# Kernel optimization log

Measured on AMD Instinct MI355X. Metric: run time of the kernel, lower is better.

Reference implementation:

```python
import jax, jax.numpy as jnp
import numpy as np

A, C, V, G = 100000, 230, 800, 60          # athletes, countries, events, games
H, HEADS, DH = 128, 4, 32                   # hidden, gat heads, per-head dim (H = HEADS*DH)
E_AC, E_AE, E_AG, E_EG = 100000, 500000, 300000, 2000
NEG_SLOPE = 0.2


def _seg_mean(msg, idx, n):
    s = jax.ops.segment_sum(msg, idx, num_segments=n)
    cnt = jax.ops.segment_sum(jnp.ones((idx.shape[0], 1), msg.dtype), idx, num_segments=n)
    return s / jnp.maximum(cnt, 1.0)


def _sage(xs, xd, ei, Wl, bl, Wr):
    # PyG SAGEConv(mean): lin_l(mean_neighbors) + lin_r(x_dst); bias lives in lin_l
    agg = _seg_mean(xs[ei[0]], ei[1], xd.shape[0])
    return agg @ Wl + bl + xd @ Wr


def _gatv2(xs, xd, ei, Wl, bl, Wr, br, att, bias):
    # PyG GATv2Conv, concat=True, add_self_loops=False, eval mode (no dropout)
    n = xd.shape[0]
    xl = (xs @ Wl + bl).reshape(-1, HEADS, DH)   # [Ns,H,d]
    xr = (xd @ Wr + br).reshape(-1, HEADS, DH)   # [Nd,H,d]
    src, dst = ei[0], ei[1]
    e = jax.nn.leaky_relu(xl[src] + xr[dst], NEG_SLOPE)      # [E,H,d]
    logit = jnp.einsum('ehd,hd->eh', e, att)                 # [E,H]
    m = jax.ops.segment_max(logit, dst, num_segments=n)
    m = jnp.where(jnp.isneginf(m), 0.0, m)                   # empty dst segments
    ex = jnp.exp(logit - m[dst])
    den = jax.ops.segment_sum(ex, dst, num_segments=n)
    alpha = ex / (den[dst] + 1e-16)
    out = jax.ops.segment_sum(xl[src] * alpha[:, :, None], dst, num_segments=n)
    return out.reshape(n, HEADS * DH) + bias


def _mlp(x, W1, b1, W2, b2):
    return jax.nn.relu(x @ W1 + b1) @ W2 + b2


def _forward(x_athlete, x_country, x_event, x_games,
             eAW1, eAb1, eAW2, eAb2, eCW1, eCb1, eCW2, eCb2,
             eEW1, eEb1, eEW2, eEb2, eGW1, eGb1, eGW2, eGb2,
             sage_Wl, sage_bl, sage_Wr,
             gat_Wl, gat_bl, gat_Wr, gat_br, gat_att, gat_bias,
             ei_ac, ei_ae, ei_ag, ei_eg):
    x = {
        'athlete': _mlp(x_athlete, eAW1, eAb1, eAW2, eAb2),
        'country': _mlp(x_country, eCW1, eCb1, eCW2, eCb2),
        'event':   _mlp(x_event,   eEW1, eEb1, eEW2, eEb2),
        'games':   _mlp(x_games,   eGW1, eGb1, eGW2, eGb2),
    }
    rev = lambda ei: ei[::-1]
    etypes = [
        ('athlete', 'country', ei_ac), ('country', 'athlete', rev(ei_ac)),
        ('athlete', 'event',   ei_ae), ('event',   'athlete', rev(ei_ae)),
        ('athlete', 'games',   ei_ag), ('games',   'athlete', rev(ei_ag)),
        ('event',   'games',   ei_eg), ('games',   'event',   rev(ei_eg)),
    ]
    # layer 1: hetero SAGEConv, HeteroConv aggr='mean' over edge types per dst
    outs = {t: [] for t in x}
    for k, (s, d, ei) in enumerate(etypes):
        outs[d].append(_sage(x[s], x[d], ei, sage_Wl[k], sage_bl[k], sage_Wr[k]))
    x = {t: jax.nn.relu(sum(o) / len(o)) for t, o in outs.items()}
    # layer 2 (final): hetero GATv2Conv, mean over edge types per dst
    outs = {t: [] for t in x}
    for k, (s, d, ei) in enumerate(etypes):
        outs[d].append(_gatv2(x[s], x[d], ei, gat_Wl[k], gat_bl[k], gat_Wr[k],
                              gat_br[k], gat_att[k], gat_bias[k]))
    x = {t: sum(o) / len(o) for t, o in outs.items()}
    return jnp.concatenate([x['athlete'], x['country'], x['event'], x['games']], axis=0)


def setup_inputs() -> dict:
    key = jax.random.key(0)
    ks = iter(jax.random.split(key, 80))
    def nrm(shape, scale=1.0):
        return jax.random.normal(next(ks), shape, jnp.float32) * scale
    def lin(fi, fo):
        return nrm((fi, fo), 1.0 / np.sqrt(fi))
    def edges(ns, nd, E):
        s = jax.random.randint(next(ks), (E,), 0, ns)
        d = jax.random.randint(next(ks), (E,), 0, nd)
        return jnp.stack([s, d]).astype(jnp.int32)
    sc = 1.0 / np.sqrt(H)
    return {
        'x_athlete': nrm((A, 7)), 'x_country': nrm((C, 3)),
        'x_event': nrm((V, 384)), 'x_games': nrm((G, 2)),
        'ei_ac': edges(A, C, E_AC), 'ei_ae': edges(A, V, E_AE),
        'ei_ag': edges(A, G, E_AG), 'ei_eg': edges(V, G, E_EG),
        'eAW1': lin(7, H),   'eAb1': jnp.zeros((H,)), 'eAW2': lin(H, H), 'eAb2': jnp.zeros((H,)),
        'eCW1': lin(3, H),   'eCb1': jnp.zeros((H,)), 'eCW2': lin(H, H), 'eCb2': jnp.zeros((H,)),
        'eEW1': lin(384, H), 'eEb1': jnp.zeros((H,)), 'eEW2': lin(H, H), 'eEb2': jnp.zeros((H,)),
        'eGW1': lin(2, H),   'eGb1': jnp.zeros((H,)), 'eGW2': lin(H, H), 'eGb2': jnp.zeros((H,)),
        'sage_Wl': nrm((8, H, H), sc), 'sage_bl': jnp.zeros((8, H)), 'sage_Wr': nrm((8, H, H), sc),
        'gat_Wl': nrm((8, H, H), sc), 'gat_bl': jnp.zeros((8, H)),
        'gat_Wr': nrm((8, H, H), sc), 'gat_br': jnp.zeros((8, H)),
        'gat_att': nrm((8, HEADS, DH), 1.0 / np.sqrt(DH)), 'gat_bias': jnp.zeros((8, H)),
    }


def reference(x_athlete, x_country, x_event, x_games,
              eAW1, eAb1, eAW2, eAb2, eCW1, eCb1, eCW2, eCb2,
              eEW1, eEb1, eEW2, eEb2, eGW1, eGb1, eGW2, eGb2,
              sage_Wl, sage_bl, sage_Wr,
              gat_Wl, gat_bl, gat_Wr, gat_br, gat_att, gat_bias,
              ei_ac, ei_ae, ei_ag, ei_eg):
    return _forward(x_athlete, x_country, x_event, x_games,
                    eAW1, eAb1, eAW2, eAb2, eCW1, eCb1, eCW2, eCb2,
                    eEW1, eEb1, eEW2, eEb2, eGW1, eGb1, eGW2, eGb2,
                    sage_Wl, sage_bl, sage_Wr,
                    gat_Wl, gat_bl, gat_Wr, gat_br, gat_att, gat_bias,
                    ei_ac, ei_ae, ei_ag, ei_eg)
```

## Files before the change

kernel.cpp:

```cpp
#include <hip/hip_runtime.h>
#include <hip/hip_bf16.h>

#define A_N 100000
#define C_N 230
#define V_N 800
#define G_N 60

#define FLAG_RELU 2

#define SCAN_N   302080
#define SCAN_NB  295
#define E_TOTAL  1804000

#define PCHUNK 16

typedef __attribute__((ext_vector_type(8))) short short8;
typedef __attribute__((ext_vector_type(4))) float f32x4;

__device__ __forceinline__ float bf16dec(unsigned short u){
  return __uint_as_float(((unsigned)u) << 16);
}
__device__ __forceinline__ unsigned short f2b(float v){
  union { __hip_bfloat16 h; unsigned short u; } c;
  c.h = __float2bfloat16(v);
  return c.u;
}
__device__ __forceinline__ float4 ldb4(const unsigned short* p){
  uint2 v = *(const uint2*)p;
  float4 r;
  r.x = __uint_as_float(v.x << 16);
  r.y = __uint_as_float(v.x & 0xffff0000u);
  r.z = __uint_as_float(v.y << 16);
  r.w = __uint_as_float(v.y & 0xffff0000u);
  return r;
}
static inline int imin(int a, int b){ return a < b ? a : b; }

__global__ void detect_dtype(const unsigned short* __restrict__ p, int* __restrict__ flag){
  __shared__ int bad;
  if (threadIdx.x == 0) bad = 0;
  __syncthreads();
  for (int i = threadIdx.x; i < 2048; i += blockDim.x){
    float v = fabsf(bf16dec(p[i]));
    if (!(v <= 1e6f)) atomicOr(&bad, 1);
  }
  __syncthreads();
  if (threadIdx.x == 0) *flag = bad;
}

struct ConvTab { const void* src[29]; int dstoff[29]; int cum[30]; };

__global__ void convert_all(ConvTab tab, float* __restrict__ wsf,
                            const int* __restrict__ flagp, int total){
  const int f = *flagp;
  for (int idx = blockIdx.x*blockDim.x + threadIdx.x; idx < total;
       idx += gridDim.x*blockDim.x){
    int t = 0;
    while (idx >= tab.cum[t+1]) ++t;
    int l = idx - tab.cum[t];
    float v = f ? ((const float*)tab.src[t])[l]
                : bf16dec(((const unsigned short*)tab.src[t])[l]);
    wsf[tab.dstoff[t] + l] = v;
  }
}

__global__ void prep_combos(const float* __restrict__ sWr, const float* __restrict__ sbl,
                            const float* __restrict__ gbias,
                            const float* __restrict__ gbl, const float* __restrict__ gbr,
                            float* __restrict__ wrcomb, float* __restrict__ sbcomb,
                            float* __restrict__ gbcomb,
                            float* __restrict__ gblx, float* __restrict__ gbrx){
  const int sets[4][3] = {{1,3,5},{0,-1,-1},{2,7,-1},{4,6,-1}};
  const float inv[4] = {1.f/3.f, 1.f, 0.5f, 0.5f};
  int idx = blockIdx.x*blockDim.x + threadIdx.x;
  if (idx >= 4*16384) return;
  int t = idx >> 14, j = idx & 16383;
  float s = 0.f;
  #pragma unroll
  for (int q = 0; q < 3; ++q){
    int k = sets[t][q];
    if (k >= 0) s += sWr[k*16384 + j];
  }
  wrcomb[idx] = s * inv[t];
  if (j < 128){
    float b1 = 0.f, b2 = 0.f;
    #pragma unroll
    for (int q = 0; q < 3; ++q){
      int k = sets[t][q];
      if (k >= 0){ b1 += sbl[k*128 + j]; b2 += gbias[k*128 + j]; }
    }
    sbcomb[t*128 + j] = b1 * inv[t];
    gbcomb[t*128 + j] = b2 * inv[t];
  }
  if (idx < 384){
    const int kl[3] = {0,2,4}, kr[3] = {1,3,5};
    int rel = idx >> 7, jj = idx & 127;
    gblx[idx] = gbl[kl[rel]*128 + jj];
// ... 155 lines not shown
__global__ void enc_batch(const float* __restrict__ wsf, unsigned short* __restrict__ wsu,
                          EncTab t){
  for (int idx = blockIdx.x*blockDim.x + threadIdx.x; idx < t.cum[4];
       idx += gridDim.x*blockDim.x){
    int s = 0;
    while (idx >= t.cum[s+1]) ++s;
    int local = idx - t.cum[s];
    if (s < 3){
      int r = local >> 7, c = local & 127;
      int K = t.K[s];
      float acc = wsf[t.boff[s] + c];
      for (int k = 0; k < K; ++k)
        acc = fmaf(wsf[t.xoff[s] + r*K + k], wsf[t.woff[s] + (k<<7) + c], acc);
      wsu[(size_t)t.zoff[s] + (size_t)r*128 + c] = f2b(fmaxf(acc, 0.f));
    } else {
      wsu[(size_t)t.zoff[3] + local] = f2b(wsf[t.xoff[3] + local]);
    }
  }
}

__device__ __forceinline__ void mfma_core(
    const unsigned short* __restrict__ wsu, const float* __restrict__ wsf,
    int xoff, int xstride, int x2off, int x2stride, int kcsplit,
    int woff, int nkc, int biasoff, int yoff, int ystride,
    int M, int flags, int mblk, int nblk)
{
  int tid = threadIdx.x;
  int wv = tid >> 6, lane = tid & 63;
  int quad = lane >> 4, ml = lane & 15;
  int m0 = mblk*64 + wv*16;
  if (m0 >= M) return;
  int arow = m0 + ml;
  bool rowok = arow < M;
  f32x4 acc[8];
  #pragma unroll
  for (int i = 0; i < 8; ++i) acc[i] = (f32x4){0.f, 0.f, 0.f, 0.f};
  for (int kc = 0; kc < nkc; ++kc){
    short8 a = (short8){0,0,0,0,0,0,0,0};
    if (rowok){
      size_t ao = (kc < kcsplit)
        ? (size_t)xoff  + (size_t)arow*xstride  + kc*32 + quad*8
        : (size_t)x2off + (size_t)arow*x2stride + (kc - kcsplit)*32 + quad*8;
      a = *(const short8*)(wsu + ao);
    }
    size_t wbase = (size_t)woff + ((size_t)(nblk*8)*nkc + kc)*512 + lane*8;
    #pragma unroll
    for (int nt = 0; nt < 8; ++nt){
      short8 b = *(const short8*)(wsu + wbase + (size_t)nt*nkc*512);
      acc[nt] = __builtin_amdgcn_mfma_f32_16x16x32_bf16(a, b, acc[nt], 0, 0, 0);
    }
  }
  #pragma unroll
  for (int nt = 0; nt < 8; ++nt){
    int col = nblk*128 + nt*16 + ml;
    float bv = (biasoff >= 0) ? wsf[biasoff + col] : 0.f;
    #pragma unroll
    for (int r = 0; r < 4; ++r){
      int orow = m0 + quad*4 + r;
      if (orow < M){
        float v = acc[nt][r] + bv;
        if (flags & FLAG_RELU) v = fmaxf(v, 0.f);
        *((unsigned short*)wsu + (size_t)yoff + (size_t)orow*ystride + col) = f2b(v);
      }
    }
  }
}

struct GB2 { int xoff, xstride, x2off, x2stride, kcsplit, woff, nkc, biasoff,
             yoff, ystride, M, flags, nblk; };
struct GB2Tab { GB2 d[13]; int b0[14]; int n; };

__global__ __launch_bounds__(256) void mfma_gemm_b2(void* ws, GB2Tab t){
  int b = blockIdx.x, di = 0;
  while (b >= t.b0[di+1]) ++di;
  GB2 g = t.d[di];
  mfma_core((const unsigned short*)ws, (const float*)ws, g.xoff, g.xstride,
            g.x2off, g.x2stride, g.kcsplit, g.woff, g.nkc, g.biasoff,
            g.yoff, g.ystride, g.M, g.flags, b - t.b0[di], g.nblk);
}

struct SgD { int src, sstr, rpoff, aggoff, nd, nc; };
struct SgTab { SgD d[5]; int cumw[6]; };

__global__ void sage_all(const unsigned short* __restrict__ wsu, float* __restrict__ wsf,
    const int* __restrict__ csr, const int* __restrict__ rpb, SgTab t,
    int uhC, int uhE, int uhG, int rp1, int rp3, int rp5, int uagg)
{
  int gid = (blockIdx.x*blockDim.x + threadIdx.x) >> 6;
  int lane = threadIdx.x & 63;
  int half = lane >> 5, sub = lane & 31, f = sub*4;
  if (gid < A_N){
    int srcs[3] = {uhC, uhE, uhG};
    int sstr[3] = {256, 384, 384};
    int rps[3]  = {rp1, rp3, rp5};
    #pragma unroll
    for (int rel = 0; rel < 3; ++rel){
      const unsigned short* base = wsu + (size_t)srcs[rel] + f;
      int str = sstr[rel];
      int st = rpb[rps[rel] + gid], en = rpb[rps[rel] + gid + 1];
      float4 acc = {0.f, 0.f, 0.f, 0.f};
      int i = st + half;
      for (; i + 2 < en; i += 4){
        int s0 = csr[i], s1 = csr[i+2];
        float4 v0 = ldb4(base + (size_t)s0*str);
        float4 v1 = ldb4(base + (size_t)s1*str);
        acc.x += v0.x + v1.x; acc.y += v0.y + v1.y;
        acc.z += v0.z + v1.z; acc.w += v0.w + v1.w;
      }
      if (i < en){
        float4 v0 = ldb4(base + (size_t)csr[i]*str);
        acc.x += v0.x; acc.y += v0.y; acc.z += v0.z; acc.w += v0.w;
      }
      acc.x += __shfl_xor(acc.x, 32); acc.y += __shfl_xor(acc.y, 32);
      acc.z += __shfl_xor(acc.z, 32); acc.w += __shfl_xor(acc.w, 32);
      if (half == 0){
        int deg = en - st;
        float sc = 1.f / (float)(deg > 1 ? deg : 1);
        ushort4 o;
        o.x = f2b(acc.x*sc); o.y = f2b(acc.y*sc);
        o.z = f2b(acc.z*sc); o.w = f2b(acc.w*sc);
        *(ushort4*)((unsigned short*)wsu + (size_t)uagg + (size_t)gid*384 + rel*128 + f) = o;
      }
    }
  } else {
    int wid = gid - A_N;
    if (wid >= t.cumw[5]) return;
    int di = 0;
    while (wid >= t.cumw[di+1]) ++di;
    SgD d = t.d[di];
    int local = wid - t.cumw[di];
    int row = local / d.nc, c = local - row*d.nc;
    const unsigned short* base = wsu + (size_t)d.src + f;
    int st = rpb[d.rpoff + row], en = rpb[d.rpoff + row + 1];
    float4 acc = {0.f, 0.f, 0.f, 0.f};
    int i = st + c + half*d.nc;
    int step = 2*d.nc;
    for (; i + step < en; i += 2*step){
      int s0 = csr[i], s1 = csr[i+step];
      float4 v0 = ldb4(base + (size_t)s0*d.sstr);
      float4 v1 = ldb4(base + (size_t)s1*d.sstr);
      acc.x += v0.x + v1.x; acc.y += v0.y + v1.y;
      acc.z += v0.z + v1.z; acc.w += v0.w + v1.w;
    }
    if (i < en){
      float4 v0 = ldb4(base + (size_t)csr[i]*d.sstr);
      acc.x += v0.x; acc.y += v0.y; acc.z += v0.z; acc.w += v0.w;
    }
    acc.x += __shfl_xor(acc.x, 32); acc.y += __shfl_xor(acc.y, 32);
    acc.z += __shfl_xor(acc.z, 32); acc.w += __shfl_xor(acc.w, 32);
    if (half == 0){
      float* o = wsf + (size_t)d.aggoff + (size_t)row*128 + f;
      atomicAdd(o,   acc.x); atomicAdd(o+1, acc.y);
      atomicAdd(o+2, acc.z); atomicAdd(o+3, acc.w);
    }
  }
}

struct AfD { int aggoff, rpoff, dstu, dstr, nd; };
struct AfTab { AfD d[5]; int n; };

__global__ void aggfin_batch(unsigned short* __restrict__ wsu, const float* __restrict__ wsf,
                             const int* __restrict__ rpb, AfTab t, int total){
  int idx = blockIdx.x*blockDim.x + threadIdx.x;
  if (idx >= total) return;
  int di = 0, local = idx;
  while (local >= t.d[di].nd*128){ local -= t.d[di].nd*128; ++di; }
  AfD d = t.d[di];
  int row = local >> 7, col = local & 127;
  int deg = rpb[d.rpoff + row + 1] - rpb[d.rpoff + row];
  float sc = 1.f / (float)(deg > 1 ? deg : 1);
  wsu[(size_t)d.dstu + (size_t)row*d.dstr + col] = f2b(wsf[(size_t)d.aggoff + local] * sc);
}

#define GAT_LOGIT(xv, pout)                                                \
  {                                                                        \
    float e0 = (xv).x + xrv.x, e1 = (xv).y + xrv.y;                        \
    float e2 = (xv).z + xrv.z, e3 = (xv).w + xrv.w;                        \
    e0 = e0 > 0.f ? e0 : 0.2f*e0; e1 = e1 > 0.f ? e1 : 0.2f*e1;            \
    e2 = e2 > 0.f ? e2 : 0.2f*e2; e3 = e3 > 0.f ? e3 : 0.2f*e3;            \
    pout = e0*av.x + e1*av.y + e2*av.z + e3*av.w;                          \
    pout += __shfl_xor(pout, 1); pout += __shfl_xor(pout, 2);              \
    pout += __shfl_xor(pout, 4);                                           \
  }

#define GAT_UPD(xv)                                                        \
  {                                                                        \
    float p;                                                               \
    GAT_LOGIT(xv, p);                                                      \
    float nm = fmaxf(m, p);                                                \
    float scw = __expf(m - nm);                                            \
    float pe = __expf(p - nm);                                             \
    l = l*scw + pe;                                                        \
    acc.x = acc.x*scw + pe*(xv).x; acc.y = acc.y*scw + pe*(xv).y;          \
    acc.z = acc.z*scw + pe*(xv).z; acc.w = acc.w*scw + pe*(xv).w;          \
    m = nm;                                                                \
  }

#define GAT_UPD2(x0, x1)                                                   \
  {                                                                        \
    float p0, p1;                                                          \
    GAT_LOGIT(x0, p0);                                                     \
    GAT_LOGIT(x1, p1);                                                     \
    float nm = fmaxf(m, fmaxf(p0, p1));                                    \
    float scw = __expf(m - nm);                                            \
    float pe0 = __expf(p0 - nm);                                           \
    float pe1 = __expf(p1 - nm);                                           \
    l = l*scw + pe0 + pe1;                                                 \
    acc.x = acc.x*scw + pe0*(x0).x + pe1*(x1).x;                           \
    acc.y = acc.y*scw + pe0*(x0).y + pe1*(x1).y;                           \
    acc.z = acc.z*scw + pe0*(x0).z + pe1*(x1).z;                           \
    acc.w = acc.w*scw + pe0*(x0).w + pe1*(x1).w;                           \
    m = nm;                                                                \
  }

#define GAT_MERGE_HALVES                                                   \
  {                                                                        \
    float mo = __shfl_xor(m, 32);                                          \
    float lo = __shfl_xor(l, 32);                                          \
    float4 ao;                                                             \
    ao.x = __shfl_xor(acc.x, 32); ao.y = __shfl_xor(acc.y, 32);            \
    ao.z = __shfl_xor(acc.z, 32); ao.w = __shfl_xor(acc.w, 32);            \
    float nm = fmaxf(m, mo);                                               \
    float w  = (m  == -INFINITY) ? 0.f : __expf(m  - nm);                  \
    float wo = (mo == -INFINITY) ? 0.f : __expf(mo - nm);                  \
    l = l*w + lo*wo;                                                       \
    acc.x = acc.x*w + ao.x*wo; acc.y = acc.y*w + ao.y*wo;                  \
    acc.z = acc.z*w + ao.z*wo; acc.w = acc.w*w + ao.w*wo;                  \
    m = nm;                                                                \
  }

__global__ void gat_ath(const unsigned short* __restrict__ wsu, const float* __restrict__ wsf,
    const int* __restrict__ csr, const int* __restrict__ rpb,
    int ugxr, int uxl1, int uxl3, int uxl5, int oatt, int rp1, int rp3, int rp5, int uout)
{
  int gid = (blockIdx.x*blockDim.x + threadIdx.x) >> 6;
  if (gid >= A_N) return;
  int lane = threadIdx.x & 63;
  int half = lane >> 5, sub = lane & 31, f = sub*4;
  int xls[3] = {uxl1, uxl3, uxl5};
  int rps[3] = {rp1, rp3, rp5};
  const int attk[3] = {1, 3, 5};
  float4 oacc = {0.f, 0.f, 0.f, 0.f};
  #pragma unroll
  for (int rel = 0; rel < 3; ++rel){
    float4 xrv = ldb4(wsu + (size_t)ugxr + (size_t)gid*384 + rel*128 + f);
    float4 av  = *(const float4*)(wsf + oatt + attk[rel]*128 + f);
    const unsigned short* base = wsu + (size_t)xls[rel] + f;
    int st = rpb[rps[rel] + gid], en = rpb[rps[rel] + gid + 1];
    float m = -INFINITY, l = 0.f;
    float4 acc = {0.f, 0.f, 0.f, 0.f};
    int i = st + half;
    for (; i + 2 < en; i += 4){
      int s0 = csr[i], s1 = csr[i+2];
      float4 x0 = ldb4(base + (size_t)s0*128);
      float4 x1 = ldb4(base + (size_t)s1*128);
      GAT_UPD2(x0, x1);
    }
    if (i < en){
      float4 x0 = ldb4(base + (size_t)csr[i]*128);
      GAT_UPD(x0);
    }
    GAT_MERGE_HALVES;
    float inv = 1.f / (l + 1e-16f);
    oacc.x += acc.x * inv; oacc.y += acc.y * inv;
    oacc.z += acc.z * inv; oacc.w += acc.w * inv;
  }
  if (half == 0){
    ushort4 o;
    o.x = f2b(oacc.x * (1.f/3.f)); o.y = f2b(oacc.y * (1.f/3.f));
    o.z = f2b(oacc.z * (1.f/3.f)); o.w = f2b(oacc.w * (1.f/3.f));
    *(ushort4*)((unsigned short*)wsu + (size_t)uout + (size_t)gid*128 + f) = o;
  }
}

struct GoD { int xl, xlstr, xr, attoff, rpoff, prefix, nd, nc; };
struct GoTab { GoD d[5]; int cumw[6]; };

__global__ void gat_online_batch(const unsigned short* __restrict__ wsu,
    const float* __restrict__ wsf, const int* __restrict__ csr,
    const int* __restrict__ rpb, float* __restrict__ part, GoTab t)
{
  int gid = (blockIdx.x*blockDim.x + threadIdx.x) >> 6;
  if (gid >= t.cumw[5]) return;
  int di = 0;
  while (gid >= t.cumw[di+1]) ++di;
  GoD d = t.d[di];
  int local = gid - t.cumw[di];
  int row = local / d.nc, c = local - row*d.nc;
  int lane = threadIdx.x & 63;
  int half = lane >> 5, sub = lane & 31, f = sub*4, h = sub >> 3;
  float4 xrv = ldb4(wsu + (size_t)d.xr + (size_t)row*128 + f);
  float4 av  = *(const float4*)(wsf + d.attoff + f);
  const unsigned short* base = wsu + (size_t)d.xl + f;
  int st = rpb[d.rpoff + row], en = rpb[d.rpoff + row + 1];
  float m = -INFINITY, l = 0.f;
  float4 acc = {0.f, 0.f, 0.f, 0.f};
  int i = st + c + half*d.nc;
  int step = 2*d.nc;
  for (; i + step < en; i += 2*step){
    int s0 = csr[i], s1 = csr[i+step];
    float4 x0 = ldb4(base + (size_t)s0*d.xlstr);
    float4 x1 = ldb4(base + (size_t)s1*d.xlstr);
    GAT_UPD2(x0, x1);
  }
  if (i < en){
    float4 x0 = ldb4(base + (size_t)csr[i]*d.xlstr);
    GAT_UPD(x0);
  }
  GAT_MERGE_HALVES;
  if (half == 0){
    float* pr = part + (size_t)(d.prefix + local)*136;
    if ((sub & 7) == 0){ pr[h] = m; pr[4+h] = l; }
    *(float4*)(pr + 8 + f) = acc;
  }
}

struct MgD { int prefix, outoff, nd, nc; float invS; };
struct MgTab { MgD d[5]; int cumw[6]; };

__global__ void gat_merge_batch(const float* __restrict__ part, float* __restrict__ wsf,
                                MgTab t){
  int gid = (blockIdx.x*blockDim.x + threadIdx.x) >> 6;
  if (gid >= t.cumw[5]) return;
  int di = 0;
  while (gid >= t.cumw[di+1]) ++di;
  MgD d = t.d[di];
  int row = gid - t.cumw[di];
  int lane = threadIdx.x & 63, f = lane*2, h = lane >> 4;
  float M = -INFINITY;
  for (int c = 0; c < d.nc; ++c)
    M = fmaxf(M, part[(size_t)(d.prefix + row*d.nc + c)*136 + h]);
  float L = 0.f;
  float2 acc = {0.f, 0.f};
  for (int c = 0; c < d.nc; ++c){
    const float* pr = part + (size_t)(d.prefix + row*d.nc + c)*136;
    float mc = pr[h];
    float w = (mc == -INFINITY) ? 0.f : __expf(mc - M);
    L += pr[4+h] * w;
    acc.x += pr[8+f]   * w;
    acc.y += pr[8+f+1] * w;
  }
  float inv = d.invS / (L + 1e-16f);
  float* o = wsf + (size_t)d.outoff + (size_t)row*128 + f;
  o[0] = acc.x * inv;
  o[1] = acc.y * inv;
}

__global__ void final_out(const unsigned short* __restrict__ wsu,
  const float* __restrict__ wsf, int uoutA, int oC0, int oE2, int oE7, int oG4, int oG6,
  int ogb, const int* __restrict__ flagp, void* __restrict__ dout)
{
  const int fl = *flagp;
  int idx = blockIdx.x*blockDim.x + threadIdx.x;
  const int total = 101090*128;
// ... 165 lines not shown
  for (int i = 0; i < 5; ++i) push(o_gWl + xlk[i]*16384, 128, u_smW[i], 4, 0, 0, 1.f);
  const int xrk[5] = {0,2,4,6,7};
  for (int i = 0; i < 5; ++i) push(o_gWr + xrk[i]*16384, 128, u_smW[5+i], 4, 0, 0, 1.f);
  st.n = sn; st.total = stotal;
  swz_batch<<<(stotal + 255)/256, 256, 0, stream>>>(wsf, wsu, st);

  hipMemsetAsync(wsf + o_cnt, 0, (size_t)SCAN_N*4, stream);
  {
    HTab ht; PTab pt;
    int hb = 0, pb = 0;
    for (int k = 0; k < 8; ++k){
      int E = et_E[k], nd = n_nodes[et_dst[k]];
      int small = (nd <= 800);
      ht.dp[k] = edp[k]; ht.E[k] = E; ht.cntoff[k] = rowbase[k];
      ht.ndst[k] = nd; ht.mode[k] = small;
      ht.bstart[k] = hb;
      hb += small ? imin(128, (E + 255)/256) : (E + 255)/256;
      pt.sp[k] = esp[k]; pt.dp[k] = edp[k]; pt.E[k] = E;
      pt.woffoff[k] = rowbase[k]; pt.ndst[k] = nd; pt.mode[k] = small;
      pt.bstart[k] = pb;
      pb += small ? imin(128, (E + 256*PCHUNK - 1)/(256*PCHUNK)) : (E + 255)/256;
    }
    ht.bstart[8] = hb; pt.bstart[8] = pb;
    hist_all<<<hb, 256, 0, stream>>>(ht, (int*)(wsf + o_cnt));
    scan1<<<SCAN_NB, 256, 0, stream>>>((int*)(wsf + o_cnt), rpb_p, (int*)(wsf + o_bsum));
    scan2<<<1, 512, 0, stream>>>((int*)(wsf + o_bsum));
    scan3<<<(SCAN_N + 255)/256, 256, 0, stream>>>(rpb_p, (int*)(wsf + o_woff),
                                                  (int*)(wsf + o_bsum));
    place_all<<<pb, 256, 0, stream>>>(pt, (int*)(wsf + o_woff), csr_p);
  }

  {
    EncTab et2;
    et2.cum[0] = 0;
    et2.cum[1] = A_N*128;
    et2.cum[2] = et2.cum[1] + C_N*128;
    et2.cum[3] = et2.cum[2] + G_N*128;
    et2.cum[4] = et2.cum[3] + 307200;
    et2.xoff[0] = coff[0]; et2.woff[0] = coff[4];  et2.boff[0] = coff[5];
    et2.zoff[0] = u_big0;  et2.K[0] = 7;
    et2.xoff[1] = coff[1]; et2.woff[1] = coff[8];  et2.boff[1] = coff[9];
    et2.zoff[1] = u_zC;    et2.K[1] = 3;
    et2.xoff[2] = coff[3]; et2.woff[2] = coff[16]; et2.boff[2] = coff[17];
    et2.zoff[2] = u_zG;    et2.K[2] = 2;
    et2.xoff[3] = coff[2]; et2.woff[3] = 0; et2.boff[3] = 0;
    et2.zoff[3] = u_xEb;   et2.K[3] = 0;
    enc_batch<<<(et2.cum[4] + 255)/256, 256, 0, stream>>>(wsf, wsu, et2);
  }

  auto pushG = [&](GB2Tab& T, GB2 g){
    T.d[T.n] = g;
    T.b0[T.n + 1] = T.b0[T.n] + (g.M + 63)/64;
    T.n++;
  };

  {
    GB2Tab t; t.n = 0; t.b0[0] = 0;
    pushG(t, GB2{u_zC, 128, 0,0,1000, u_eCW2, 4, coff[11], u_sxC, 256, C_N, 0, 0});
    pushG(t, GB2{u_xEb, 384, 0,0,1000, u_eEW1, 12, coff[13], u_zE, 128, V_N, FLAG_RELU, 0});
    pushG(t, GB2{u_zG, 128, 0,0,1000, u_eGW2, 4, coff[19], u_sxG, 384, G_N, 0, 0});
    pushG(t, GB2{u_big0, 128, 0,0,1000, u_eAW2, 4, coff[7], u_bigH, 128, A_N, 0, 0});
    mfma_gemm_b2<<<t.b0[t.n], 256, 0, stream>>>(d_ws, t);
  }
  {
    GB2Tab t; t.n = 0; t.b0[0] = 0;
    pushG(t, GB2{u_zE, 128, 0,0,1000, u_eEW2, 4, coff[15], u_sxE, 384, V_N, 0, 0});
    mfma_gemm_b2<<<t.b0[t.n], 256, 0, stream>>>(d_ws, t);
  }

  hipMemsetAsync(wsf + o_aggS, 0, (size_t)1950*128*4, stream);
  const int b0 = o_aggS, b2 = o_aggS + 230*128, b7 = b2 + 800*128,
            b4 = b7 + 800*128, b6 = b4 + 60*128;
  SgTab sg;
  sg.d[0] = SgD{u_bigH, 128, rowbase[0], b0, C_N, 32};
  sg.d[1] = SgD{u_bigH, 128, rowbase[2], b2, V_N, 16};
  sg.d[2] = SgD{u_sxG, 384, rowbase[7], b7, V_N, 8};
  sg.d[3] = SgD{u_bigH, 128, rowbase[4], b4, G_N, 128};
  sg.d[4] = SgD{u_sxE, 384, rowbase[6], b6, G_N, 32};
  sg.cumw[0] = 0;
  {
    int c = 0;
    for (int i = 0; i < 5; ++i){ c += sg.d[i].nd*sg.d[i].nc; sg.cumw[i+1] = c; }
  }
  {
    int waves = A_N + sg.cumw[5];
    sage_all<<<(waves*64 + 255)/256, 256, 0, stream>>>(wsu, wsf, csr_p, rpb_p, sg,
        u_sxC, u_sxE, u_sxG, rowbase[1], rowbase[3], rowbase[5], u_bigA);
  }
  AfTab af; af.n = 5;
  af.d[0] = AfD{b0, rowbase[0], u_sxC + 128, 256, C_N};
  af.d[1] = AfD{b2, rowbase[2], u_sxE + 128, 384, V_N};
  af.d[2] = AfD{b7, rowbase[7], u_sxE + 256, 384, V_N};
  af.d[3] = AfD{b4, rowbase[4], u_sxG + 128, 384, G_N};
  af.d[4] = AfD{b6, rowbase[6], u_sxG + 256, 384, G_N};
  int aftot = 1950*128;
  aggfin_batch<<<(aftot + 255)/256, 256, 0, stream>>>(wsu, wsf, rpb_p, af, aftot);

  {
    GB2Tab t; t.n = 0; t.b0[0] = 0;
    pushG(t, GB2{u_sxC, 256, 0,0,1000, u_sxCW, 8,  o_sbcomb + 128, u_yC, 128, C_N, FLAG_RELU, 0});
    pushG(t, GB2{u_sxE, 384, 0,0,1000, u_sxEW, 12, o_sbcomb + 256, u_yE, 128, V_N, FLAG_RELU, 0});
    pushG(t, GB2{u_sxG, 384, 0,0,1000, u_sxGW, 12, o_sbcomb + 384, u_yG, 128, G_N, FLAG_RELU, 0});
    pushG(t, GB2{u_bigH, 128, u_bigA, 384, 4, u_sxAW, 16, o_sbcomb, u_big0, 128, A_N, FLAG_RELU, 0});
    mfma_gemm_b2<<<t.b0[t.n], 256, 0, stream>>>(d_ws, t);
  }

  {
    GB2Tab t; t.n = 0; t.b0[0] = 0;
    pushG(t, GB2{u_big0, 128, 0,0,1000, u_gxlW, 4, o_gblx, u_bigA, 384, A_N, 0, 0});
    pushG(t, GB2{u_big0, 128, 0,0,1000, u_gxlW, 4, o_gblx, u_bigA, 384, A_N, 0, 1});
    pushG(t, GB2{u_big0, 128, 0,0,1000, u_gxlW, 4, o_gblx, u_bigA, 384, A_N, 0, 2});
    pushG(t, GB2{u_yC, 128, 0,0,1000, u_smW[0], 4, o_gbl + 1*128, u_xl1, 128, C_N, 0, 0});
    pushG(t, GB2{u_yE, 128, 0,0,1000, u_smW[1], 4, o_gbl + 3*128, u_xl3, 128, V_N, 0, 0});
    pushG(t, GB2{u_yG, 128, 0,0,1000, u_smW[2], 4, o_gbl + 5*128, u_xl5, 128, G_N, 0, 0});
    pushG(t, GB2{u_yE, 128, 0,0,1000, u_smW[3], 4, o_gbl + 6*128, u_xl6, 128, V_N, 0, 0});
    pushG(t, GB2{u_yG, 128, 0,0,1000, u_smW[4], 4, o_gbl + 7*128, u_xl7, 128, G_N, 0, 0});
    pushG(t, GB2{u_yC, 128, 0,0,1000, u_smW[5], 4, o_gbr + 0*128, u_xr0, 128, C_N, 0, 0});
    pushG(t, GB2{u_yE, 128, 0,0,1000, u_smW[6], 4, o_gbr + 2*128, u_xr2, 128, V_N, 0, 0});
    pushG(t, GB2{u_yG, 128, 0,0,1000, u_smW[7], 4, o_gbr + 4*128, u_xr4, 128, G_N, 0, 0});
    pushG(t, GB2{u_yG, 128, 0,0,1000, u_smW[8], 4, o_gbr + 6*128, u_xr6, 128, G_N, 0, 0});
    pushG(t, GB2{u_yE, 128, 0,0,1000, u_smW[9], 4, o_gbr + 7*128, u_xr7, 128, V_N, 0, 0});
    mfma_gemm_b2<<<t.b0[t.n], 256, 0, stream>>>(d_ws, t);
  }

  GoTab go;
  go.d[0] = GoD{u_bigA + 0,   384, u_xr0, o_gatt + 0*128, rowbase[0], 0,     C_N, 32};
  go.d[1] = GoD{u_bigA + 128, 384, u_xr2, o_gatt + 2*128, rowbase[2], 7360,  V_N, 16};
  go.d[2] = GoD{u_bigA + 256, 384, u_xr4, o_gatt + 4*128, rowbase[4], 20160, G_N, 128};
  go.d[3] = GoD{u_xl6, 128,        u_xr6, o_gatt + 6*128, rowbase[6], 27840, G_N, 32};
  go.d[4] = GoD{u_xl7, 128,        u_xr7, o_gatt + 7*128, rowbase[7], 29760, V_N, 8};
  go.cumw[0] = 0;
  {
    int c = 0;
    for (int i = 0; i < 5; ++i){ c += go.d[i].nd*go.d[i].nc; go.cumw[i+1] = c; }
  }
  gat_online_batch<<<(go.cumw[5]*64 + 255)/256, 256, 0, stream>>>(wsu, wsf, csr_p, rpb_p,
      wsf + o_part, go);

  {
    GB2Tab t; t.n = 0; t.b0[0] = 0;
    pushG(t, GB2{u_big0, 128, 0,0,1000, u_gxrW, 4, o_gbrx, u_bigA, 384, A_N, 0, 0});
    pushG(t, GB2{u_big0, 128, 0,0,1000, u_gxrW, 4, o_gbrx, u_bigA, 384, A_N, 0, 1});
    pushG(t, GB2{u_big0, 128, 0,0,1000, u_gxrW, 4, o_gbrx, u_bigA, 384, A_N, 0, 2});
    mfma_gemm_b2<<<t.b0[t.n], 256, 0, stream>>>(d_ws, t);
  }
  gat_ath<<<(A_N*64 + 255)/256, 256, 0, stream>>>(wsu, wsf, csr_p, rpb_p,
      u_bigA, u_xl1, u_xl3, u_xl5, o_gatt, rowbase[1], rowbase[3], rowbase[5], u_bigH);

  MgTab mg;
  mg.d[0] = MgD{0,     o_outC0, C_N, 32,  1.0f};
  mg.d[1] = MgD{7360,  o_outE2, V_N, 16,  0.5f};
  mg.d[2] = MgD{20160, o_outG4, G_N, 128, 0.5f};
  mg.d[3] = MgD{27840, o_outG6, G_N, 32,  0.5f};
  mg.d[4] = MgD{29760, o_outE7, V_N, 8,   0.5f};
  mg.cumw[0] = 0;
  {
    int c = 0;
    for (int i = 0; i < 5; ++i){ c += mg.d[i].nd; mg.cumw[i+1] = c; }
  }
  gat_merge_batch<<<(mg.cumw[5]*64 + 255)/256, 256, 0, stream>>>(wsf + o_part, wsf, mg);

  final_out<<<(101090*128 + 255)/256, 256, 0, stream>>>(wsu, wsf, u_bigH,
      o_outC0, o_outE2, o_outE7, o_outG4, o_outG6, o_gbcomb, flagp, d_out);
}
```

Measured before the change: 1.021 ms.

## Fuse athlete SAGE aggregation and GAT xr projection into their consumer kernels

The athlete-side SAGE mean aggregation now writes into LDS and is followed in the same kernel by the MFMA GEMM that produces the athlete hidden state. This avoids the global round trip through the aggregation buffer and the separate GEMM launch. Likewise, the GATv2 xr projection for athletes is computed per 64-row block into LDS inside the attention kernel rather than by a separate GEMM. The cost is one wave per 16 rows doing serial gathers, lower occupancy from about 50KB of LDS per block, and per-block reloading of the weights.

```diff
diff --git a/kernel.cpp b/kernel.cpp
--- a/kernel.cpp
+++ b/kernel.cpp
@@ -13,6 +13,7 @@
 #define E_TOTAL  1804000
 
 #define PCHUNK 16
+#define LROW 392
 
 typedef __attribute__((ext_vector_type(8))) short short8;
 typedef __attribute__((ext_vector_type(4))) float f32x4;
@@ -334,22 +335,81 @@
 struct SgD { int src, sstr, rpoff, aggoff, nd, nc; };
 struct SgTab { SgD d[5]; int cumw[6]; };
 
-__global__ void sage_all(const unsigned short* __restrict__ wsu, float* __restrict__ wsf,
-    const int* __restrict__ csr, const int* __restrict__ rpb, SgTab t,
-    int uhC, int uhE, int uhG, int rp1, int rp3, int rp5, int uagg)
+__global__ void sage_small(const unsigned short* __restrict__ wsu, float* __restrict__ wsf,
+    const int* __restrict__ csr, const int* __restrict__ rpb, SgTab t)
 {
   int gid = (blockIdx.x*blockDim.x + threadIdx.x) >> 6;
+  if (gid >= t.cumw[5]) return;
   int lane = threadIdx.x & 63;
   int half = lane >> 5, sub = lane & 31, f = sub*4;
-  if (gid < A_N){
-    int srcs[3] = {uhC, uhE, uhG};
-    int sstr[3] = {256, 384, 384};
-    int rps[3]  = {rp1, rp3, rp5};
+  int di = 0;
+  while (gid >= t.cumw[di+1]) ++di;
+  SgD d = t.d[di];
+  int local = gid - t.cumw[di];
+  int row = local / d.nc, c = local - row*d.nc;
+  const unsigned short* base = wsu + (size_t)d.src + f;
+  int st = rpb[d.rpoff + row], en = rpb[d.rpoff + row + 1];
+  float4 acc = {0.f, 0.f, 0.f, 0.f};
+  int i = st + c + half*d.nc;
+  int step = 2*d.nc;
+  for (; i + step < en; i += 2*step){
+    int s0 = csr[i], s1 = csr[i+step];
+    float4 v0 = ldb4(base + (size_t)s0*d.sstr);
+    float4 v1 = ldb4(base + (size_t)s1*d.sstr);
+    acc.x += v0.x + v1.x; acc.y += v0.y + v1.y;
+    acc.z += v0.z + v1.z; acc.w += v0.w + v1.w;
+  }
+  if (i < en){
+    float4 v0 = ldb4(base + (size_t)csr[i]*d.sstr);
+    acc.x += v0.x; acc.y += v0.y; acc.z += v0.z; acc.w += v0.w;
+  }
+  acc.x += __shfl_xor(acc.x, 32); acc.y += __shfl_xor(acc.y, 32);
+  acc.z += __shfl_xor(acc.z, 32); acc.w += __shfl_xor(acc.w, 32);
+  if (half == 0){
+    float* o = wsf + (size_t)d.aggoff + (size_t)row*128 + f;
+    atomicAdd(o,   acc.x); atomicAdd(o+1, acc.y);
+    atomicAdd(o+2, acc.z); atomicAdd(o+3, acc.w);
+  }
+}
+
+struct AfD { int aggoff, rpoff, dstu, dstr, nd; };
+struct AfTab { AfD d[5]; int n; };
+
+__global__ void aggfin_batch(unsigned short* __restrict__ wsu, const float* __restrict__ wsf,
+                             const int* __restrict__ rpb, AfTab t, int total){
+  int idx = blockIdx.x*blockDim.x + threadIdx.x;
+  if (idx >= total) return;
+  int di = 0, local = idx;
+  while (local >= t.d[di].nd*128){ local -= t.d[di].nd*128; ++di; }
+  AfD d = t.d[di];
+  int row = local >> 7, col = local & 127;
+  int deg = rpb[d.rpoff + row + 1] - rpb[d.rpoff + row];
+  float sc = 1.f / (float)(deg > 1 ? deg : 1);
+  wsu[(size_t)d.dstu + (size_t)row*d.dstr + col] = f2b(wsf[(size_t)d.aggoff + local] * sc);
+}
+
+__global__ __launch_bounds__(256) void sage_ath_fused(
+    unsigned short* __restrict__ wsu, const float* __restrict__ wsf,
+    const int* __restrict__ csr, const int* __restrict__ rpb,
+    int uhC, int uhE, int uhG, int rp1, int rp3, int rp5,
+    int uhA, int woff, int biasoff, int yoff)
+{
+  __shared__ unsigned short lds[64*LROW];
+  int tid = threadIdx.x;
+  int wv = tid >> 6, lane = tid & 63;
+  int half = lane >> 5, sub = lane & 31, f = sub*4;
+  int m0 = blockIdx.x*64;
+  int srcs[3] = {uhC, uhE, uhG};
+  int sstr[3] = {256, 384, 384};
+  int rps[3]  = {rp1, rp3, rp5};
+  for (int r = 0; r < 16; ++r){
+    int row = m0 + wv*16 + r;
+    if (row >= A_N) break;
     #pragma unroll
     for (int rel = 0; rel < 3; ++rel){
       const unsigned short* base = wsu + (size_t)srcs[rel] + f;
       int str = sstr[rel];
-      int st = rpb[rps[rel] + gid], en = rpb[rps[rel] + gid + 1];
+      int st = rpb[rps[rel] + row], en = rpb[rps[rel] + row + 1];
       float4 acc = {0.f, 0.f, 0.f, 0.f};
       int i = st + half;
       for (; i + 2 < en; i += 4){
@@ -371,57 +431,42 @@
         ushort4 o;
         o.x = f2b(acc.x*sc); o.y = f2b(acc.y*sc);
         o.z = f2b(acc.z*sc); o.w = f2b(acc.w*sc);
-        *(ushort4*)((unsigned short*)wsu + (size_t)uagg + (size_t)gid*384 + rel*128 + f) = o;
+        *(ushort4*)&lds[(wv*16 + r)*LROW + rel*128 + f] = o;
       }
     }
-  } else {
-    int wid = gid - A_N;
-    if (wid >= t.cumw[5]) return;
-    int di = 0;
-    while (wid >= t.cumw[di+1]) ++di;
-    SgD d = t.d[di];
-    int local = wid - t.cumw[di];
-    int row = local / d.nc, c = local - row*d.nc;
-    const unsigned short* base = wsu + (size_t)d.src + f;
-    int st = rpb[d.rpoff + row], en = rpb[d.rpoff + row + 1];
-    float4 acc = {0.f, 0.f, 0.f, 0.f};
-    int i = st + c + half*d.nc;
-    int step = 2*d.nc;
-    for (; i + step < en; i += 2*step){
-      int s0 = csr[i], s1 = csr[i+step];
-      float4 v0 = ldb4(base + (size_t)s0*d.sstr);
-      float4 v1 = ldb4(base + (size_t)s1*d.sstr);
-      acc.x += v0.x + v1.x; acc.y += v0.y + v1.y;
-      acc.z += v0.z + v1.z; acc.w += v0.w + v1.w;
-    }
-    if (i < en){
-      float4 v0 = ldb4(base + (size_t)csr[i]*d.sstr);
-      acc.x += v0.x; acc.y += v0.y; acc.z += v0.z; acc.w += v0.w;
-    }
-    acc.x += __shfl_xor(acc.x, 32); acc.y += __shfl_xor(acc.y, 32);
-    acc.z += __shfl_xor(acc.z, 32); acc.w += __shfl_xor(acc.w, 32);
-    if (half == 0){
-      float* o = wsf + (size_t)d.aggoff + (size_t)row*128 + f;
-      atomicAdd(o,   acc.x); atomicAdd(o+1, acc.y);
-      atomicAdd(o+2, acc.z); atomicAdd(o+3, acc.w);
-    }
-  }
-}
-
-struct AfD { int aggoff, rpoff, dstu, dstr, nd; };
-struct AfTab { AfD d[5]; int n; };
-
-__global__ void aggfin_batch(unsigned short* __restrict__ wsu, const float* __restrict__ wsf,
-                             const int* __restrict__ rpb, AfTab t, int total){
-  int idx = blockIdx.x*blockDim.x + threadIdx.x;
-  if (idx >= total) return;
-  int di = 0, local = idx;
-  while (local >= t.d[di].nd*128){ local -= t.d[di].nd*128; ++di; }
-  AfD d = t.d[di];
-  int row = local >> 7, col = local & 127;
-  int deg = rpb[d.rpoff + row + 1] - rpb[d.rpoff + row];
-  float sc = 1.f / (float)(deg > 1 ? deg : 1);
-  wsu[(size_t)d.dstu + (size_t)row*d.dstr + col] = f2b(wsf[(size_t)d.aggoff + local] * sc);
+  }
+  __syncthreads();
+  int quad = lane >> 4, ml = lane & 15;
+  if (m0 + wv*16 >= A_N) return;
+  int arow = m0 + wv*16 + ml;
+  bool rowok = arow < A_N;
+  f32x4 acc[8];
+  #pragma unroll
+  for (int i = 0; i < 8; ++i) acc[i] = (f32x4){0.f, 0.f, 0.f, 0.f};
+  for (int kc = 0; kc < 16; ++kc){
+    short8 a = (short8){0,0,0,0,0,0,0,0};
+    if (rowok){
+      if (kc < 4) a = *(const short8*)(wsu + (size_t)uhA + (size_t)arow*128 + kc*32 + quad*8);
+      else        a = *(const short8*)&lds[(wv*16 + ml)*LROW + (kc-4)*32 + quad*8];
+    }
+    size_t wbase = (size_t)woff + (size_t)kc*512 + lane*8;
+    #pragma unroll
+    for (int nt = 0; nt < 8; ++nt){
+      short8 b = *(const short8*)(wsu + wbase + (size_t)nt*16*512);
+      acc[nt] = __builtin_amdgcn_mfma_f32_16x16x32_bf16(a, b, acc[nt], 0, 0, 0);
+    }
+  }
+  #pragma unroll
+  for (int nt = 0; nt < 8; ++nt){
+    int col = nt*16 + ml;
+    float bv = wsf[biasoff + col];
+    #pragma unroll
+    for (int r = 0; r < 4; ++r){
+      int orow = m0 + wv*16 + quad*4 + r;
+      if (orow < A_N)
+        wsu[(size_t)yoff + (size_t)orow*128 + col] = f2b(fmaxf(acc[nt][r] + bv, 0.f));
+    }
+  }
 }
 
 #define GAT_LOGIT(xv, pout)                                                \
@@ -481,47 +526,85 @@
     m = nm;                                                                \
   }
 
-__global__ void gat_ath(const unsigned short* __restrict__ wsu, const float* __restrict__ wsf,
+__global__ __launch_bounds__(256) void gat_ath_fused(
+    unsigned short* __restrict__ wsu, const float* __restrict__ wsf,
     const int* __restrict__ csr, const int* __restrict__ rpb,
-    int ugxr, int uxl1, int uxl3, int uxl5, int oatt, int rp1, int rp3, int rp5, int uout)
+    int uyA, int woff, int biasoff,
+    int uxl1, int uxl3, int uxl5, int oatt, int rp1, int rp3, int rp5, int uout)
 {
-  int gid = (blockIdx.x*blockDim.x + threadIdx.x) >> 6;
-  if (gid >= A_N) return;
-  int lane = threadIdx.x & 63;
+  __shared__ unsigned short lds[64*LROW];
+  int tid = threadIdx.x;
+  int wv = tid >> 6, lane = tid & 63;
+  int quad = lane >> 4, ml = lane & 15;
+  int m0 = blockIdx.x*64;
+  {
+    int arow = m0 + wv*16 + ml;
+    bool rowok = arow < A_N;
+    for (int nb = 0; nb < 3; ++nb){
+      f32x4 acc[8];
+      #pragma unroll
+      for (int i = 0; i < 8; ++i) acc[i] = (f32x4){0.f, 0.f, 0.f, 0.f};
+      for (int kc = 0; kc < 4; ++kc){
+        short8 a = (short8){0,0,0,0,0,0,0,0};
+        if (rowok) a = *(const short8*)(wsu + (size_t)uyA + (size_t)arow*128 + kc*32 + quad*8);
+        size_t wbase = (size_t)woff + ((size_t)(nb*8)*4 + kc)*512 + lane*8;
+        #pragma unroll
+        for (int nt = 0; nt < 8; ++nt){
+          short8 b = *(const short8*)(wsu + wbase + (size_t)nt*4*512);
+          acc[nt] = __builtin_amdgcn_mfma_f32_16x16x32_bf16(a, b, acc[nt], 0, 0, 0);
+        }
+      }
+      #pragma unroll
+      for (int nt = 0; nt < 8; ++nt){
+        int col = nb*128 + nt*16 + ml;
+        float bv = wsf[biasoff + col];
+        #pragma unroll
+        for (int r = 0; r < 4; ++r){
+          int lrow = wv*16 + quad*4 + r;
+          lds[lrow*LROW + col] = f2b(acc[nt][r] + bv);
+        }
+      }
+    }
+  }
+  __syncthreads();
   int half = lane >> 5, sub = lane & 31, f = sub*4;
   int xls[3] = {uxl1, uxl3, uxl5};
   int rps[3] = {rp1, rp3, rp5};
   const int attk[3] = {1, 3, 5};
-  float4 oacc = {0.f, 0.f, 0.f, 0.f};
-  #pragma unroll
-  for (int rel = 0; rel < 3; ++rel){
-    float4 xrv = ldb4(wsu + (size_t)ugxr + (size_t)gid*384 + rel*128 + f);
-    float4 av  = *(const float4*)(wsf + oatt + attk[rel]*128 + f);
-    const unsigned short* base = wsu + (size_t)xls[rel] + f;
-    int st = rpb[rps[rel] + gid], en = rpb[rps[rel] + gid + 1];
-    float m = -INFINITY, l = 0.f;
-    float4 acc = {0.f, 0.f, 0.f, 0.f};
-    int i = st + half;
-    for (; i + 2 < en; i += 4){
-      int s0 = csr[i], s1 = csr[i+2];
-      float4 x0 = ldb4(base + (size_t)s0*128);
-      float4 x1 = ldb4(base + (size_t)s1*128);
-      GAT_UPD2(x0, x1);
-    }
-    if (i < en){
-      float4 x0 = ldb4(base + (size_t)csr[i]*128);
-      GAT_UPD(x0);
-    }
-    GAT_MERGE_HALVES;
-    float inv = 1.f / (l + 1e-16f);
-    oacc.x += acc.x * inv; oacc.y += acc.y * inv;
-    oacc.z += acc.z * inv; oacc.w += acc.w * inv;
-  }
-  if (half == 0){
-    ushort4 o;
-    o.x = f2b(oacc.x * (1.f/3.f)); o.y = f2b(oacc.y * (1.f/3.f));
-    o.z = f2b(oacc.z * (1.f/3.f)); o.w = f2b(oacc.w * (1.f/3.f));
-    *(ushort4*)((unsigned short*)wsu + (size_t)uout + (size_t)gid*128 + f) = o;
+  for (int r = 0; r < 16; ++r){
+    int row = m0 + wv*16 + r;
+    if (row >= A_N) break;
+    float4 oacc = {0.f, 0.f, 0.f, 0.f};
+    #pragma unroll
+    for (int rel = 0; rel < 3; ++rel){
+      float4 xrv = ldb4(&lds[(wv*16 + r)*LROW + rel*128 + f]);
+      float4 av  = *(const float4*)(wsf + oatt + attk[rel]*128 + f);
+      const unsigned short* base = wsu + (size_t)xls[rel] + f;
+      int st = rpb[rps[rel] + row], en = rpb[rps[rel] + row + 1];
+      float m = -INFINITY, l = 0.f;
+      float4 acc = {0.f, 0.f, 0.f, 0.f};
+      int i = st + half;
+      for (; i + 2 < en; i += 4){
+        int s0 = csr[i], s1 = csr[i+2];
+        float4 x0 = ldb4(base + (size_t)s0*128);
+        float4 x1 = ldb4(base + (size_t)s1*128);
+        GAT_UPD2(x0, x1);
+      }
+      if (i < en){
+        float4 x0 = ldb4(base + (size_t)csr[i]*128);
+        GAT_UPD(x0);
+      }
+      GAT_MERGE_HALVES;
+      float inv = 1.f / (l + 1e-16f);
+      oacc.x += acc.x * inv; oacc.y += acc.y * inv;
+      oacc.z += acc.z * inv; oacc.w += acc.w * inv;
+    }
+    if (half == 0){
+      ushort4 o;
+      o.x = f2b(oacc.x * (1.f/3.f)); o.y = f2b(oacc.y * (1.f/3.f));
+      o.z = f2b(oacc.z * (1.f/3.f)); o.w = f2b(oacc.w * (1.f/3.f));
+      *(ushort4*)((unsigned short*)wsu + (size_t)uout + (size_t)row*128 + f) = o;
+    }
   }
 }
 
@@ -853,11 +936,7 @@
     int c = 0;
     for (int i = 0; i < 5; ++i){ c += sg.d[i].nd*sg.d[i].nc; sg.cumw[i+1] = c; }
   }
-  {
-    int waves = A_N + sg.cumw[5];
-    sage_all<<<(waves*64 + 255)/256, 256, 0, stream>>>(wsu, wsf, csr_p, rpb_p, sg,
-        u_sxC, u_sxE, u_sxG, rowbase[1], rowbase[3], rowbase[5], u_bigA);
-  }
+  sage_small<<<(sg.cumw[5]*64 + 255)/256, 256, 0, stream>>>(wsu, wsf, csr_p, rpb_p, sg);
   AfTab af; af.n = 5;
   af.d[0] = AfD{b0, rowbase[0], u_sxC + 128, 256, C_N};
   af.d[1] = AfD{b2, rowbase[2], u_sxE + 128, 384, V_N};
@@ -872,9 +951,11 @@
     pushG(t, GB2{u_sxC, 256, 0,0,1000, u_sxCW, 8,  o_sbcomb + 128, u_yC, 128, C_N, FLAG_RELU, 0});
     pushG(t, GB2{u_sxE, 384, 0,0,1000, u_sxEW, 12, o_sbcomb + 256, u_yE, 128, V_N, FLAG_RELU, 0});
     pushG(t, GB2{u_sxG, 384, 0,0,1000, u_sxGW, 12, o_sbcomb + 384, u_yG, 128, G_N, FLAG_RELU, 0});
-    pushG(t, GB2{u_bigH, 128, u_bigA, 384, 4, u_sxAW, 16, o_sbcomb, u_big0, 128, A_N, FLAG_RELU, 0});
     mfma_gemm_b2<<<t.b0[t.n], 256, 0, stream>>>(d_ws, t);
   }
+  sage_ath_fused<<<(A_N + 63)/64, 256, 0, stream>>>(wsu, wsf, csr_p, rpb_p,
+      u_sxC, u_sxE, u_sxG, rowbase[1], rowbase[3], rowbase[5],
+      u_bigH, u_sxAW, o_sbcomb, u_big0);
 
   {
     GB2Tab t; t.n = 0; t.b0[0] = 0;
@@ -908,15 +989,9 @@
   gat_online_batch<<<(go.cumw[5]*64 + 255)/256, 256, 0, stream>>>(wsu, wsf, csr_p, rpb_p,
       wsf + o_part, go);
 
-  {
-    GB2Tab t; t.n = 0; t.b0[0] = 0;
-    pushG(t, GB2{u_big0, 128, 0,0,1000, u_gxrW, 4, o_gbrx, u_bigA, 384, A_N, 0, 0});
-    pushG(t, GB2{u_big0, 128, 0,0,1000, u_gxrW, 4, o_gbrx, u_bigA, 384, A_N, 0, 1});
-    pushG(t, GB2{u_big0, 128, 0,0,1000, u_gxrW, 4, o_gbrx, u_bigA, 384, A_N, 0, 2});
-    mfma_gemm_b2<<<t.b0[t.n], 256, 0, stream>>>(d_ws, t);
-  }
-  gat_ath<<<(A_N*64 + 255)/256, 256, 0, stream>>>(wsu, wsf, csr_p, rpb_p,
-      u_bigA, u_xl1, u_xl3, u_xl5, o_gatt, rowbase[1], rowbase[3], rowbase[5], u_bigH);
+  gat_ath_fused<<<(A_N + 63)/64, 256, 0, stream>>>(wsu, wsf, csr_p, rpb_p,
+      u_big0, u_gxrW, o_gbrx, u_xl1, u_xl3, u_xl5, o_gatt,
+      rowbase[1], rowbase[3], rowbase[5], u_bigH);
 
   MgTab mg;
   mg.d[0] = MgD{0,     o_outC0, C_N, 32,  1.0f};
```

Result: slower. 1.064 ms (+4.3%).
